# Kernel tuning notes

Measured on AMD Instinct MI355X. Metric: run time of the kernel, lower is better.

## Reference

```python
import math
import jax, jax.numpy as jnp
import numpy as np

B, S, E = 4, 2048, 1024

def setup_inputs() -> dict:
    key = jax.random.key(0)
    k1, k2, k3 = jax.random.split(key, 3)
    X = jax.random.normal(k1, (B, S, E), dtype=jnp.float32)
    # nn.Linear(E, 3E): weight [3E, E], bias [3E]; scale weights for sane softmax
    W = jax.random.normal(k2, (3 * E, E), dtype=jnp.float32) * (1.0 / math.sqrt(E))
    b = jax.random.normal(k3, (3 * E,), dtype=jnp.float32) * 0.01
    return {"X": X, "W": W, "b": b}

def reference(X, W, b):
    E_ = X.shape[-1]
    # fused QKV projection: X @ W^T + b -> [B, S, 3E]
    qkv = jnp.einsum('bse,fe->bsf', X, W) + b
    q, k, v = jnp.split(qkv, 3, axis=-1)
    scores = jnp.einsum('bqe,bke->bqk', q, k) / math.sqrt(E_)
    attention_weight = jax.nn.softmax(scores, axis=-1)  # [B, S, S]
    output = jnp.einsum('bqk,bke->bqe', attention_weight, v)
    return (output, attention_weight)
```

## Files before the change

### kernel.cpp

```cpp
#include <hip/hip_runtime.h>
#include <math.h>

typedef __bf16 bf16;
typedef __bf16 bf16x4 __attribute__((ext_vector_type(4)));
typedef __bf16 bf16x8 __attribute__((ext_vector_type(8)));
typedef float f32x4 __attribute__((ext_vector_type(4)));

#define MODE_QKV    0
#define MODE_SCORES 1
#define MODE_PV     2

__device__ inline void gload_lds16(const bf16* g, bf16* l) {
    __builtin_amdgcn_global_load_lds(
        (const __attribute__((address_space(1))) void*)g,
        (__attribute__((address_space(3))) void*)l, 16, 0, 0);
}

template <int MODE>
__global__ __launch_bounds__(256) void mfma_nt(
    const bf16* __restrict__ A, const bf16* __restrict__ B,
    const float* __restrict__ bias, void* __restrict__ Cv,
    bf16* __restrict__ Vt, float* __restrict__ lsum,
    int K, int lda, int ldb, int ldc,
    long sA, long sB, long sC, float alpha)
{
    A += (long)blockIdx.z * sA;
    B += (long)blockIdx.z * sB;
    char* Cb = (char*)Cv + (long)blockIdx.z * sC;
    if constexpr (MODE != MODE_QKV) lsum += (long)blockIdx.z * 2048;

    __shared__ bf16 As[128 * 32] __attribute__((aligned(16)));
    __shared__ bf16 Bs[128 * 32] __attribute__((aligned(16)));

    const int t  = threadIdx.x;
    const int m0 = blockIdx.y * 128;
    const int n0 = blockIdx.x * 128;

    const int lane = t & 63;
    const int wave = t >> 6;
    const int wrow = (wave >> 1) * 64;
    const int wcol = (wave & 1) * 64;
    const int fr   = lane & 15;
    const int kq   = (lane >> 4) * 8;

    const int r0 = t >> 2,           k80 = (t & 3) * 8;
    const int r1 = (t + 256) >> 2,   k81 = ((t + 256) & 3) * 8;

    f32x4 acc[4][4] = {};

    for (int k0 = 0; k0 < K; k0 += 32) {
        gload_lds16(A + (long)(m0 + r0) * lda + k0 + k80, &As[t * 8]);
        gload_lds16(A + (long)(m0 + r1) * lda + k0 + k81, &As[(t + 256) * 8]);
        gload_lds16(B + (long)(n0 + r0) * ldb + k0 + k80, &Bs[t * 8]);
        gload_lds16(B + (long)(n0 + r1) * ldb + k0 + k81, &Bs[(t + 256) * 8]);
        __syncthreads();

        bf16x8 af[4], bfr[4];
#pragma unroll
        for (int i = 0; i < 4; i++) {
            af[i]  = *(const bf16x8*)&As[(wrow + i * 16 + fr) * 32 + kq];
            bfr[i] = *(const bf16x8*)&Bs[(wcol + i * 16 + fr) * 32 + kq];
        }
#pragma unroll
        for (int i = 0; i < 4; i++)
#pragma unroll
            for (int j = 0; j < 4; j++)
                acc[i][j] = __builtin_amdgcn_mfma_f32_16x16x32_bf16(
                    af[i], bfr[j], acc[i][j], 0, 0, 0);
        __syncthreads();
    }

    const int r4 = (lane >> 4) * 4;

    if constexpr (MODE == MODE_QKV) {
        if (n0 >= 2048) {
#pragma unroll
            for (int j = 0; j < 4; j++) {
                const int col = n0 + wcol + j * 16 + fr;
                const float bv = bias[col];
                const int e = col - 2048;
#pragma unroll
                for (int i = 0; i < 4; i++) {
                    const int row = m0 + wrow + i * 16 + r4;
                    const int b = row >> 11, s = row & 2047;
                    bf16x4 pk;
#pragma unroll
                    for (int r = 0; r < 4; r++) pk[r] = (bf16)(acc[i][j][r] + bv);
                    *(bf16x4*)(Vt + ((long)b * 1024 + e) * 2048 + s) = pk;
                }
            }
        } else {
            bf16* C = (bf16*)Cb;
#pragma unroll
            for (int j = 0; j < 4; j++) {
                const int col = n0 + wcol + j * 16 + fr;
                const float bv = bias[col];
#pragma unroll
                for (int i = 0; i < 4; i++)
#pragma unroll
                    for (int r = 0; r < 4; r++) {
                        const long row = m0 + wrow + i * 16 + r4 + r;
                        C[row * ldc + col] = (bf16)(acc[i][j][r] + bv);
                    }
            }
        }
    } else if constexpr (MODE == MODE_SCORES) {
        bf16* C = (bf16*)Cb;
        float rsum[4][4];
#pragma unroll
        for (int i = 0; i < 4; i++)
#pragma unroll
            for (int r = 0; r < 4; r++) rsum[i][r] = 0.f;
#pragma unroll
        for (int j = 0; j < 4; j++) {
            const int col = n0 + wcol + j * 16 + fr;
#pragma unroll
            for (int i = 0; i < 4; i++)
#pragma unroll
                for (int r = 0; r < 4; r++) {
                    const long row = m0 + wrow + i * 16 + r4 + r;
                    const float e = __expf(alpha * acc[i][j][r]);
                    C[row * ldc + col] = (bf16)e;
                    rsum[i][r] += e;
                }
        }
#pragma unroll
        for (int off = 1; off < 16; off <<= 1)
#pragma unroll
            for (int i = 0; i < 4; i++)
#pragma unroll
                for (int r = 0; r < 4; r++)
                    rsum[i][r] += __shfl_xor(rsum[i][r], off);
        if (fr == 0) {
#pragma unroll
            for (int i = 0; i < 4; i++)
#pragma unroll
                for (int r = 0; r < 4; r++)
                    atomicAdd(&lsum[m0 + wrow + i * 16 + r4 + r], rsum[i][r]);
        }
    } else {
        float* C = (float*)Cb;
        float linv[4][4];
#pragma unroll
        for (int i = 0; i < 4; i++)
#pragma unroll
            for (int r = 0; r < 4; r++)
                linv[i][r] = 1.0f / lsum[m0 + wrow + i * 16 + r4 + r];
#pragma unroll
        for (int j = 0; j < 4; j++) {
            const int col = n0 + wcol + j * 16 + fr;
#pragma unroll
            for (int i = 0; i < 4; i++)
#pragma unroll
                for (int r = 0; r < 4; r++) {
                    const long row = m0 + wrow + i * 16 + r4 + r;
                    C[row * ldc + col] = acc[i][j][r] * linv[i][r];
                }
        }
    }
}

__global__ __launch_bounds__(256) void f32_to_bf16(
    const float* __restrict__ in, bf16* __restrict__ out, long n)
{
    long i = ((long)blockIdx.x * 256 + threadIdx.x) * 4;
    if (i < n) {
        float4 v = *(const float4*)(in + i);
        bf16x4 o = { (bf16)v.x, (bf16)v.y, (bf16)v.z, (bf16)v.w };
        *(bf16x4*)(out + i) = o;
    }
}

__global__ __launch_bounds__(256) void normalize_rows(
    const bf16* __restrict__ Pu, const float* __restrict__ l,
    float* __restrict__ out1)
{
    const long row = blockIdx.x;
    const float inv = 1.0f / l[row];
    const bf16* p = Pu + row * 2048;
    float* o = out1 + row * 2048;
    const int t = threadIdx.x;
    bf16x8 v = *(const bf16x8*)(p + t * 8);
    float4 a, b;
    a.x = (float)v[0] * inv; a.y = (float)v[1] * inv;
    a.z = (float)v[2] * inv; a.w = (float)v[3] * inv;
    b.x = (float)v[4] * inv; b.y = (float)v[5] * inv;
    b.z = (float)v[6] * inv; b.w = (float)v[7] * inv;
    *(float4*)(o + t * 8)     = a;
    *(float4*)(o + t * 8 + 4) = b;
}

extern "C" void kernel_launch(void* const* d_in, const int* in_sizes, int n_in,
                              void* d_out, int out_size, void* d_ws, size_t ws_size,
                              hipStream_t stream)
{
    const int B = 4, S = 2048, E = 1024;
    const float* X    = (const float*)d_in[0];
    const float* W    = (const float*)d_in[1];
    const float* bias = (const float*)d_in[2];

    float* out0 = (float*)d_out;
    float* out1 = out0 + (long)B * S * E;

    char* ws = (char*)d_ws;
    bf16* QKb = (bf16*)(ws);
    bf16* Vt  = (bf16*)(ws + 33554432);
    bf16* Pu  = (bf16*)(ws + 50331648);
    float* l  = (float*)(ws + 83886080);
    bf16* Xb  = (bf16*)(ws + 50331648);
    bf16* Wb  = (bf16*)(ws + 67108864);

    f32_to_bf16<<<(long)B * S * E / 1024, 256, 0, stream>>>(X, Xb, (long)B * S * E);
    f32_to_bf16<<<(long)3 * E * E / 1024, 256, 0, stream>>>(W, Wb, (long)3 * E * E);
    hipMemsetAsync(l, 0, (long)B * S * sizeof(float), stream);

    mfma_nt<MODE_QKV><<<dim3(3 * E / 128, B * S / 128, 1), 256, 0, stream>>>(
        Xb, Wb, bias, QKb, Vt, nullptr,
        E, E, E, 2048, 0, 0, 0, 1.0f);

    mfma_nt<MODE_SCORES><<<dim3(S / 128, S / 128, B), 256, 0, stream>>>(
        QKb, QKb + 1024, nullptr, Pu, nullptr, l,
        E, 2048, 2048, S,
        (long)S * 2048, (long)S * 2048, (long)S * S * 2 , 0.03125f);

    normalize_rows<<<B * S, 256, 0, stream>>>(Pu, l, out1);

    mfma_nt<MODE_PV><<<dim3(E / 128, S / 128, B), 256, 0, stream>>>(
        Pu, Vt, nullptr, out0, nullptr, l,
        S, S, S, E,
        (long)S * S, (long)E * S, (long)S * E * 4 , 1.0f);
}
```

Baseline: 358.9 us.

## Switch GEMMs to 32x32x16 MFMA with k-major LDS layout and split QKV launch

```diff
diff --git a/kernel.cpp b/kernel.cpp
--- a/kernel.cpp
+++ b/kernel.cpp
@@ -4,11 +4,12 @@
 typedef __bf16 bf16;
 typedef __bf16 bf16x4 __attribute__((ext_vector_type(4)));
 typedef __bf16 bf16x8 __attribute__((ext_vector_type(8)));
-typedef float f32x4 __attribute__((ext_vector_type(4)));
-
-#define MODE_QKV    0
-#define MODE_SCORES 1
-#define MODE_PV     2
+typedef float f32x16 __attribute__((ext_vector_type(16)));
+
+#define MODE_QK     0
+#define MODE_V      1
+#define MODE_SCORES 2
+#define MODE_PV     3
 
 __device__ inline void gload_lds16(const bf16* g, bf16* l) {
     __builtin_amdgcn_global_load_lds(
@@ -27,7 +28,8 @@
     A += (long)blockIdx.z * sA;
     B += (long)blockIdx.z * sB;
     char* Cb = (char*)Cv + (long)blockIdx.z * sC;
-    if constexpr (MODE != MODE_QKV) lsum += (long)blockIdx.z * 2048;
+    if constexpr (MODE == MODE_SCORES || MODE == MODE_PV)
+        lsum += (long)blockIdx.z * 2048;
 
     __shared__ bf16 As[128 * 32] __attribute__((aligned(16)));
     __shared__ bf16 Bs[128 * 32] __attribute__((aligned(16)));
@@ -40,122 +42,139 @@
     const int wave = t >> 6;
     const int wrow = (wave >> 1) * 64;
     const int wcol = (wave & 1) * 64;
-    const int fr   = lane & 15;
-    const int kq   = (lane >> 4) * 8;
-
-    const int r0 = t >> 2,           k80 = (t & 3) * 8;
-    const int r1 = (t + 256) >> 2,   k81 = ((t + 256) & 3) * 8;
-
-    f32x4 acc[4][4] = {};
+    const int lm   = lane & 31;
+    const int khl  = lane >> 5;
+
+    const int sr0 = t & 127,        sk0 = (t >> 7) * 8;
+    const int sr1 = t & 127,        sk1 = ((t + 256) >> 7) * 8;
+
+    f32x16 acc[2][2] = {};
 
     for (int k0 = 0; k0 < K; k0 += 32) {
-        gload_lds16(A + (long)(m0 + r0) * lda + k0 + k80, &As[t * 8]);
-        gload_lds16(A + (long)(m0 + r1) * lda + k0 + k81, &As[(t + 256) * 8]);
-        gload_lds16(B + (long)(n0 + r0) * ldb + k0 + k80, &Bs[t * 8]);
-        gload_lds16(B + (long)(n0 + r1) * ldb + k0 + k81, &Bs[(t + 256) * 8]);
+        gload_lds16(A + (long)(m0 + sr0) * lda + k0 + sk0, &As[t * 8]);
+        gload_lds16(A + (long)(m0 + sr1) * lda + k0 + sk1, &As[(t + 256) * 8]);
+        gload_lds16(B + (long)(n0 + sr0) * ldb + k0 + sk0, &Bs[t * 8]);
+        gload_lds16(B + (long)(n0 + sr1) * ldb + k0 + sk1, &Bs[(t + 256) * 8]);
         __syncthreads();
 
-        bf16x8 af[4], bfr[4];
-#pragma unroll
-        for (int i = 0; i < 4; i++) {
-            af[i]  = *(const bf16x8*)&As[(wrow + i * 16 + fr) * 32 + kq];
-            bfr[i] = *(const bf16x8*)&Bs[(wcol + i * 16 + fr) * 32 + kq];
-        }
-#pragma unroll
-        for (int i = 0; i < 4; i++)
-#pragma unroll
-            for (int j = 0; j < 4; j++)
-                acc[i][j] = __builtin_amdgcn_mfma_f32_16x16x32_bf16(
-                    af[i], bfr[j], acc[i][j], 0, 0, 0);
+        bf16x8 af[2][2], bf[2][2];
+#pragma unroll
+        for (int ks = 0; ks < 2; ks++) {
+            const int kc = (ks * 2 + khl) * 128;
+#pragma unroll
+            for (int i = 0; i < 2; i++) {
+                af[ks][i] = *(const bf16x8*)&As[(kc + wrow + i * 32 + lm) * 8];
+                bf[ks][i] = *(const bf16x8*)&Bs[(kc + wcol + i * 32 + lm) * 8];
+            }
+        }
+#pragma unroll
+        for (int ks = 0; ks < 2; ks++)
+#pragma unroll
+            for (int i = 0; i < 2; i++)
+#pragma unroll
+                for (int j = 0; j < 2; j++)
+                    acc[i][j] = __builtin_amdgcn_mfma_f32_32x32x16_bf16(
+                        af[ks][i], bf[ks][j], acc[i][j], 0, 0, 0);
         __syncthreads();
     }
 
-    const int r4 = (lane >> 4) * 4;
-
-    if constexpr (MODE == MODE_QKV) {
-        if (n0 >= 2048) {
-#pragma unroll
-            for (int j = 0; j < 4; j++) {
-                const int col = n0 + wcol + j * 16 + fr;
-                const float bv = bias[col];
-                const int e = col - 2048;
-#pragma unroll
-                for (int i = 0; i < 4; i++) {
-                    const int row = m0 + wrow + i * 16 + r4;
-                    const int b = row >> 11, s = row & 2047;
+    const int rb = 4 * khl;
+
+    if constexpr (MODE == MODE_QK) {
+        bf16* C = (bf16*)Cb;
+#pragma unroll
+        for (int j = 0; j < 2; j++) {
+            const int col = n0 + wcol + j * 32 + lm;
+            const float bv = bias[col];
+#pragma unroll
+            for (int i = 0; i < 2; i++) {
+                const int base = m0 + wrow + i * 32 + rb;
+#pragma unroll
+                for (int reg = 0; reg < 16; reg++) {
+                    const long row = base + (reg & 3) + 8 * (reg >> 2);
+                    C[row * ldc + col] = (bf16)(acc[i][j][reg] + bv);
+                }
+            }
+        }
+    } else if constexpr (MODE == MODE_V) {
+#pragma unroll
+        for (int j = 0; j < 2; j++) {
+            const int e = n0 + wcol + j * 32 + lm;
+            const float bv = bias[e];
+#pragma unroll
+            for (int i = 0; i < 2; i++) {
+                const int srow = m0 + wrow + i * 32 + rb;
+                const int b = srow >> 11, s = srow & 2047;
+#pragma unroll
+                for (int q = 0; q < 4; q++) {
                     bf16x4 pk;
 #pragma unroll
-                    for (int r = 0; r < 4; r++) pk[r] = (bf16)(acc[i][j][r] + bv);
-                    *(bf16x4*)(Vt + ((long)b * 1024 + e) * 2048 + s) = pk;
-                }
-            }
-        } else {
-            bf16* C = (bf16*)Cb;
-#pragma unroll
-            for (int j = 0; j < 4; j++) {
-                const int col = n0 + wcol + j * 16 + fr;
-                const float bv = bias[col];
-#pragma unroll
-                for (int i = 0; i < 4; i++)
-#pragma unroll
-                    for (int r = 0; r < 4; r++) {
-                        const long row = m0 + wrow + i * 16 + r4 + r;
-                        C[row * ldc + col] = (bf16)(acc[i][j][r] + bv);
-                    }
+                    for (int r = 0; r < 4; r++)
+                        pk[r] = (bf16)(acc[i][j][q * 4 + r] + bv);
+                    *(bf16x4*)(Vt + ((long)b * 1024 + e) * 2048 + s + 8 * q) = pk;
+                }
             }
         }
     } else if constexpr (MODE == MODE_SCORES) {
         bf16* C = (bf16*)Cb;
-        float rsum[4][4];
-#pragma unroll
-        for (int i = 0; i < 4; i++)
-#pragma unroll
-            for (int r = 0; r < 4; r++) rsum[i][r] = 0.f;
-#pragma unroll
-        for (int j = 0; j < 4; j++) {
-            const int col = n0 + wcol + j * 16 + fr;
-#pragma unroll
-            for (int i = 0; i < 4; i++)
-#pragma unroll
-                for (int r = 0; r < 4; r++) {
-                    const long row = m0 + wrow + i * 16 + r4 + r;
-                    const float e = __expf(alpha * acc[i][j][r]);
+        float rsum[2][16];
+#pragma unroll
+        for (int i = 0; i < 2; i++)
+#pragma unroll
+            for (int reg = 0; reg < 16; reg++) rsum[i][reg] = 0.f;
+#pragma unroll
+        for (int j = 0; j < 2; j++) {
+            const int col = n0 + wcol + j * 32 + lm;
+#pragma unroll
+            for (int i = 0; i < 2; i++) {
+                const int base = m0 + wrow + i * 32 + rb;
+#pragma unroll
+                for (int reg = 0; reg < 16; reg++) {
+                    const long row = base + (reg & 3) + 8 * (reg >> 2);
+                    const float e = __expf(alpha * acc[i][j][reg]);
                     C[row * ldc + col] = (bf16)e;
-                    rsum[i][r] += e;
-                }
-        }
-#pragma unroll
-        for (int off = 1; off < 16; off <<= 1)
-#pragma unroll
-            for (int i = 0; i < 4; i++)
-#pragma unroll
-                for (int r = 0; r < 4; r++)
-                    rsum[i][r] += __shfl_xor(rsum[i][r], off);
-        if (fr == 0) {
-#pragma unroll
-            for (int i = 0; i < 4; i++)
-#pragma unroll
-                for (int r = 0; r < 4; r++)
-                    atomicAdd(&lsum[m0 + wrow + i * 16 + r4 + r], rsum[i][r]);
+                    rsum[i][reg] += e;
+                }
+            }
+        }
+#pragma unroll
+        for (int off = 1; off < 32; off <<= 1)
+#pragma unroll
+            for (int i = 0; i < 2; i++)
+#pragma unroll
+                for (int reg = 0; reg < 16; reg++)
+                    rsum[i][reg] += __shfl_xor(rsum[i][reg], off);
+        if (lm == 0) {
+#pragma unroll
+            for (int i = 0; i < 2; i++) {
+                const int base = m0 + wrow + i * 32 + rb;
+#pragma unroll
+                for (int reg = 0; reg < 16; reg++)
+                    atomicAdd(&lsum[base + (reg & 3) + 8 * (reg >> 2)], rsum[i][reg]);
+            }
         }
     } else {
         float* C = (float*)Cb;
-        float linv[4][4];
-#pragma unroll
-        for (int i = 0; i < 4; i++)
-#pragma unroll
-            for (int r = 0; r < 4; r++)
-                linv[i][r] = 1.0f / lsum[m0 + wrow + i * 16 + r4 + r];
-#pragma unroll
-        for (int j = 0; j < 4; j++) {
-            const int col = n0 + wcol + j * 16 + fr;
-#pragma unroll
-            for (int i = 0; i < 4; i++)
-#pragma unroll
-                for (int r = 0; r < 4; r++) {
-                    const long row = m0 + wrow + i * 16 + r4 + r;
-                    C[row * ldc + col] = acc[i][j][r] * linv[i][r];
-                }
+        float linv[2][16];
+#pragma unroll
+        for (int i = 0; i < 2; i++) {
+            const int base = m0 + wrow + i * 32 + rb;
+#pragma unroll
+            for (int reg = 0; reg < 16; reg++)
+                linv[i][reg] = 1.0f / lsum[base + (reg & 3) + 8 * (reg >> 2)];
+        }
+#pragma unroll
+        for (int j = 0; j < 2; j++) {
+            const int col = n0 + wcol + j * 32 + lm;
+#pragma unroll
+            for (int i = 0; i < 2; i++) {
+                const int base = m0 + wrow + i * 32 + rb;
+#pragma unroll
+                for (int reg = 0; reg < 16; reg++) {
+                    const long row = base + (reg & 3) + 8 * (reg >> 2);
+                    C[row * ldc + col] = acc[i][j][reg] * linv[i][reg];
+                }
+            }
         }
     }
 }
@@ -214,19 +233,23 @@
     f32_to_bf16<<<(long)3 * E * E / 1024, 256, 0, stream>>>(W, Wb, (long)3 * E * E);
     hipMemsetAsync(l, 0, (long)B * S * sizeof(float), stream);
 
-    mfma_nt<MODE_QKV><<<dim3(3 * E / 128, B * S / 128, 1), 256, 0, stream>>>(
-        Xb, Wb, bias, QKb, Vt, nullptr,
+    mfma_nt<MODE_QK><<<dim3(2048 / 128, B * S / 128, 1), 256, 0, stream>>>(
+        Xb, Wb, bias, QKb, nullptr, nullptr,
         E, E, E, 2048, 0, 0, 0, 1.0f);
+
+    mfma_nt<MODE_V><<<dim3(1024 / 128, B * S / 128, 1), 256, 0, stream>>>(
+        Xb, Wb + (long)2048 * 1024, bias + 2048, nullptr, Vt, nullptr,
+        E, E, E, 0, 0, 0, 0, 1.0f);
 
     mfma_nt<MODE_SCORES><<<dim3(S / 128, S / 128, B), 256, 0, stream>>>(
         QKb, QKb + 1024, nullptr, Pu, nullptr, l,
         E, 2048, 2048, S,
-        (long)S * 2048, (long)S * 2048, (long)S * S * 2 , 0.03125f);
+        (long)S * 2048, (long)S * 2048, (long)S * S * 2, 0.03125f);
 
     normalize_rows<<<B * S, 256, 0, stream>>>(Pu, l, out1);
 
     mfma_nt<MODE_PV><<<dim3(E / 128, S / 128, B), 256, 0, stream>>>(
         Pu, Vt, nullptr, out0, nullptr, l,
         S, S, S, E,
-        (long)S * S, (long)E * S, (long)S * E * 4 , 1.0f);
-}
+        (long)S * S, (long)E * S, (long)S * E * 4, 1.0f);
+}
```

New measurement: 432.7 us. +20.5%, slower.
